# Kernel optimization log

Measured on AMD Instinct MI355X. Metric: run time of the kernel, lower is better.

Reference implementation:

```python
import jax, jax.numpy as jnp
import numpy as np

N = 100000       # nodes
DEG = 16         # in-degree per node
E = N * DEG      # edges
IN_DIM = 128
H_DIM = 128
NEG_SLOPE = 0.01  # F.leaky_relu default


def setup_inputs() -> dict:
    key = jax.random.key(0)
    ks = jax.random.split(key, 12)
    sc = 0.05
    attr = jax.random.normal(ks[0], (N, IN_DIM), jnp.float32)
    edge_d = jax.random.uniform(ks[1], (E, 1), dtype=jnp.float32)
    edge_src = jax.random.randint(ks[2], (E,), 0, N, dtype=jnp.int32)
    edge_dst = jnp.repeat(jnp.arange(N, dtype=jnp.int32), DEG)  # every node gets DEG msgs
    return {
        "attr": attr,
        "edge_d": edge_d,
        "W_V1": jax.random.normal(ks[3], (1, 1), jnp.float32) * sc,
        "W_W1": jax.random.normal(ks[4], (H_DIM, IN_DIM), jnp.float32) * sc,
        "W_U1": jax.random.normal(ks[5], (H_DIM, IN_DIM), jnp.float32) * sc,
        "W_a1": jax.random.normal(ks[6], (1, 2 * H_DIM + 1), jnp.float32) * sc,
        "W_V2": jax.random.normal(ks[7], (1, 1), jnp.float32) * sc,
        "W_W2": jax.random.normal(ks[8], (H_DIM, H_DIM), jnp.float32) * sc,
        "W_U2": jax.random.normal(ks[9], (H_DIM, H_DIM), jnp.float32) * sc,
        "W_a2": jax.random.normal(ks[10], (1, 2 * H_DIM + 1), jnp.float32) * sc,
        "edge_src": edge_src,
        "edge_dst": edge_dst,
    }


def gat_layer(h, edge_d, edge_src, edge_dst, W_V, W_W, W_U, W_a):
    n = h.shape[0]
    t = edge_d @ W_V.T                      # [E,1] edge feature transform (fcV)
    z = h @ W_W.T                           # [N,H] (fcW)
    z_i = h @ W_U.T                         # [N,H] (fcU)
    Hd = z.shape[1]
    a = W_a[0]                              # [2H+1]
    a_src, a_dst, a_t = a[:Hd], a[Hd:2 * Hd], a[2 * Hd:]
    # attn_fc(concat(z_src, z_dst, t)) decomposed into per-node scores + edge term
    s_src = z @ a_src                       # [N]
    s_dst = z @ a_dst                       # [N]
    e = s_src[edge_src] + s_dst[edge_dst] + (t @ a_t)  # [E]
    e = jax.nn.leaky_relu(e, NEG_SLOPE)
    # per-destination-node softmax over incoming edges (mailbox softmax)
    m = jax.ops.segment_max(e, edge_dst, num_segments=n)
    ex = jnp.exp(e - m[edge_dst])
    denom = jax.ops.segment_sum(ex, edge_dst, num_segments=n)
    alpha = ex / denom[edge_dst]            # [E]
    # weighted neighbor aggregation
    zn = jax.ops.segment_sum(alpha[:, None] * z[edge_src], edge_dst, num_segments=n)
    return jax.nn.relu(z_i + zn)


def reference(attr, edge_d, W_V1, W_W1, W_U1, W_a1, W_V2, W_W2, W_U2, W_a2,
              edge_src, edge_dst):
    h = gat_layer(attr, edge_d, edge_src, edge_dst, W_V1, W_W1, W_U1, W_a1)
    h = gat_layer(h, edge_d, edge_src, edge_dst, W_V2, W_W2, W_U2, W_a2)
    return h
```

## Files before the change

kernel.cpp:

```cpp
#include <hip/hip_runtime.h>

#define N_NODES 100000
#define DEG 16
#define DIM 128
#define NGROUPS 6250
#define GPB 5
#define DBLOCKS (NGROUPS / GPB)

typedef short bf16x8 __attribute__((ext_vector_type(8)));
typedef float f32x4 __attribute__((ext_vector_type(4)));

__device__ __forceinline__ unsigned short f2bf(float f) {
    unsigned int u = __builtin_bit_cast(unsigned int, f);
    u = (u + 0x7fffu + ((u >> 16) & 1u)) >> 16;
    return (unsigned short)u;
}
__device__ __forceinline__ float bf2f(unsigned short h) {
    unsigned int u = ((unsigned int)h) << 16;
    return __builtin_bit_cast(float, u);
}

template <bool F32IN>
__global__ __launch_bounds__(256) void dense_fused(
    const void* __restrict__ hsrc,
    const float* __restrict__ W_W,
    const float* __restrict__ W_U,
    const float* __restrict__ W_a,
    unsigned short* __restrict__ zcat,
    float* __restrict__ s_src,
    float* __restrict__ s_dst)
{
    __shared__ float sred[2][2][2][16];

    const int wave = threadIdx.x >> 6;
    const int lane = threadIdx.x & 63;
    const int n16 = lane & 15;
    const int quad = lane >> 4;

    const float* Wbase = (wave < 2) ? (W_W + (size_t)wave * 64 * DIM)
                                    : (W_U + (size_t)(wave - 2) * 64 * DIM);
    bf16x8 wfrag[4][4];
#pragma unroll
    for (int ct = 0; ct < 4; ct++) {
        const float* wrow = Wbase + (size_t)(ct * 16 + n16) * DIM + quad * 8;
#pragma unroll
        for (int ks = 0; ks < 4; ks++) {
            float4 lo = *(const float4*)(wrow + ks * 32);
            float4 hi = *(const float4*)(wrow + ks * 32 + 4);
            bf16x8 f;
            f[0] = (short)f2bf(lo.x); f[1] = (short)f2bf(lo.y);
            f[2] = (short)f2bf(lo.z); f[3] = (short)f2bf(lo.w);
            f[4] = (short)f2bf(hi.x); f[5] = (short)f2bf(hi.y);
            f[6] = (short)f2bf(hi.z); f[7] = (short)f2bf(hi.w);
            wfrag[ct][ks] = f;
        }
    }

    float4 av_s[4], av_d[4];
    if (wave < 2) {
#pragma unroll
        for (int ct = 0; ct < 4; ct++) {
            av_s[ct] = *(const float4*)(W_a + wave * 64 + ct * 16 + quad * 4);
            av_d[ct] = *(const float4*)(W_a + DIM + wave * 64 + ct * 16 + quad * 4);
        }
    }

    for (int g = 0; g < GPB; g++) {
        const int nodebase = (blockIdx.x * GPB + g) * 16;

        bf16x8 hfrag[4];
        if (F32IN) {
            const float* hrow = (const float*)hsrc + (size_t)(nodebase + n16) * DIM + quad * 8;
#pragma unroll
            for (int ks = 0; ks < 4; ks++) {
                float4 lo = *(const float4*)(hrow + ks * 32);
                float4 hi = *(const float4*)(hrow + ks * 32 + 4);
                bf16x8 f;
                f[0] = (short)f2bf(lo.x); f[1] = (short)f2bf(lo.y);
                f[2] = (short)f2bf(lo.z); f[3] = (short)f2bf(lo.w);
                f[4] = (short)f2bf(hi.x); f[5] = (short)f2bf(hi.y);
                f[6] = (short)f2bf(hi.z); f[7] = (short)f2bf(hi.w);
                hfrag[ks] = f;
            }
        } else {
            const unsigned short* hrow = (const unsigned short*)hsrc + (size_t)(nodebase + n16) * DIM + quad * 8;
#pragma unroll
            for (int ks = 0; ks < 4; ks++)
                hfrag[ks] = *(const bf16x8*)(hrow + ks * 32);
        }

        f32x4 acc[4];
#pragma unroll
        for (int ct = 0; ct < 4; ct++) {
            f32x4 a = {0.f, 0.f, 0.f, 0.f};
#pragma unroll
            for (int ks = 0; ks < 4; ks++)
                a = __builtin_amdgcn_mfma_f32_16x16x32_bf16(wfrag[ct][ks], hfrag[ks], a, 0, 0, 0);
            acc[ct] = a;
        }

        unsigned short* orow = zcat + (size_t)(nodebase + n16) * 256 + wave * 64 + quad * 4;
#pragma unroll
        for (int ct = 0; ct < 4; ct++) {
            uint2 pk;
            pk.x = (unsigned int)f2bf(acc[ct][0]) | ((unsigned int)f2bf(acc[ct][1]) << 16);
            pk.y = (unsigned int)f2bf(acc[ct][2]) | ((unsigned int)f2bf(acc[ct][3]) << 16);
            *(uint2*)(orow + ct * 16) = pk;
        }

        if (wave < 2) {
            float ps = 0.f, pd = 0.f;
#pragma unroll
            for (int ct = 0; ct < 4; ct++) {
                ps += acc[ct][0] * av_s[ct].x + acc[ct][1] * av_s[ct].y
                    + acc[ct][2] * av_s[ct].z + acc[ct][3] * av_s[ct].w;
                pd += acc[ct][0] * av_d[ct].x + acc[ct][1] * av_d[ct].y
                    + acc[ct][2] * av_d[ct].z + acc[ct][3] * av_d[ct].w;
            }
            ps += __shfl_xor(ps, 16); ps += __shfl_xor(ps, 32);
            pd += __shfl_xor(pd, 16); pd += __shfl_xor(pd, 32);
            if (lane < 16) {
                sred[g & 1][wave][0][n16] = ps;
                sred[g & 1][wave][1][n16] = pd;
            }
        }
        __syncthreads();
        if (wave == 3) {
            if (lane < 16)
                s_src[nodebase + lane] = sred[g & 1][0][0][lane] + sred[g & 1][1][0][lane];
            else if (lane < 32)
                s_dst[nodebase + lane - 16] = sred[g & 1][0][1][lane - 16] + sred[g & 1][1][1][lane - 16];
        }
    }
}

__global__ __launch_bounds__(256) void aggr_kernel(
    const unsigned short* __restrict__ zcat,
    const float* __restrict__ s_src,
    const float* __restrict__ s_dst,
    const float* __restrict__ edge_d,
    const int* __restrict__ edge_src,
    const float* __restrict__ W_V,
    const float* __restrict__ W_a,
    unsigned short* __restrict__ out_bf16,
    float* __restrict__ out_f32)
{
    __shared__ float alpha_s[16][DEG];
    __shared__ int   src_s[16][DEG];

    const int t = threadIdx.x;
    const int base = blockIdx.x * 16;

    {
        int nl = t >> 4, j = t & 15;
        int node = base + nl;
        int e = node * DEG + j;
        int s = edge_src[e];
        float coef = W_V[0] * W_a[2 * DIM];
        float x = s_src[s] + s_dst[node] + edge_d[e] * coef;
        x = x > 0.f ? x : 0.01f * x;
        float m = x;
        m = fmaxf(m, __shfl_xor(m, 1));
        m = fmaxf(m, __shfl_xor(m, 2));
        m = fmaxf(m, __shfl_xor(m, 4));
        m = fmaxf(m, __shfl_xor(m, 8));
        float ex = __expf(x - m);
        float d = ex;
        d += __shfl_xor(d, 1); d += __shfl_xor(d, 2);
        d += __shfl_xor(d, 4); d += __shfl_xor(d, 8);
        alpha_s[nl][j] = ex / d;
        src_s[nl][j] = s;
    }
    __syncthreads();

    const int nl = t >> 4;
    const int node = base + nl;
    const int c8 = (t & 15) * 8;

    float acc[8] = {};
#pragma unroll
    for (int j = 0; j < DEG; j++) {
        int s = src_s[nl][j];
        float a = alpha_s[nl][j];
        uint4 raw = *(const uint4*)(zcat + (size_t)s * 256 + c8);
        acc[0] += a * bf2f((unsigned short)raw.x);
        acc[1] += a * bf2f((unsigned short)(raw.x >> 16));
        acc[2] += a * bf2f((unsigned short)raw.y);
        acc[3] += a * bf2f((unsigned short)(raw.y >> 16));
        acc[4] += a * bf2f((unsigned short)raw.z);
        acc[5] += a * bf2f((unsigned short)(raw.z >> 16));
        acc[6] += a * bf2f((unsigned short)raw.w);
        acc[7] += a * bf2f((unsigned short)(raw.w >> 16));
    }

    uint4 zr = *(const uint4*)(zcat + (size_t)node * 256 + 128 + c8);
    float v[8];
    v[0] = fmaxf(bf2f((unsigned short)zr.x) + acc[0], 0.f);
    v[1] = fmaxf(bf2f((unsigned short)(zr.x >> 16)) + acc[1], 0.f);
    v[2] = fmaxf(bf2f((unsigned short)zr.y) + acc[2], 0.f);
    v[3] = fmaxf(bf2f((unsigned short)(zr.y >> 16)) + acc[3], 0.f);
    v[4] = fmaxf(bf2f((unsigned short)zr.z) + acc[4], 0.f);
    v[5] = fmaxf(bf2f((unsigned short)(zr.z >> 16)) + acc[5], 0.f);
    v[6] = fmaxf(bf2f((unsigned short)zr.w) + acc[6], 0.f);
    v[7] = fmaxf(bf2f((unsigned short)(zr.w >> 16)) + acc[7], 0.f);

    if (out_f32) {
        float* op = out_f32 + (size_t)node * DIM + c8;
        *(float4*)op       = make_float4(v[0], v[1], v[2], v[3]);
        *(float4*)(op + 4) = make_float4(v[4], v[5], v[6], v[7]);
    } else {
        uint4 pk;
        pk.x = (unsigned int)f2bf(v[0]) | ((unsigned int)f2bf(v[1]) << 16);
        pk.y = (unsigned int)f2bf(v[2]) | ((unsigned int)f2bf(v[3]) << 16);
        pk.z = (unsigned int)f2bf(v[4]) | ((unsigned int)f2bf(v[5]) << 16);
        pk.w = (unsigned int)f2bf(v[6]) | ((unsigned int)f2bf(v[7]) << 16);
        *(uint4*)(out_bf16 + (size_t)node * DIM + c8) = pk;
    }
}

extern "C" void kernel_launch(void* const* d_in, const int* in_sizes, int n_in,
                              void* d_out, int out_size, void* d_ws, size_t ws_size,
                              hipStream_t stream) {
    const float* attr     = (const float*)d_in[0];
    const float* edge_d   = (const float*)d_in[1];
    const float* W_V1     = (const float*)d_in[2];
    const float* W_W1     = (const float*)d_in[3];
    const float* W_U1     = (const float*)d_in[4];
    const float* W_a1     = (const float*)d_in[5];
    const float* W_V2     = (const float*)d_in[6];
    const float* W_W2     = (const float*)d_in[7];
    const float* W_U2     = (const float*)d_in[8];
    const float* W_a2     = (const float*)d_in[9];
    const int*   edge_src = (const int*)d_in[10];

    float* out = (float*)d_out;

    char* ws = (char*)d_ws;
    unsigned short* zcat = (unsigned short*)ws;
    unsigned short* h1   = (unsigned short*)(ws + 52u * 1024 * 1024);
    float* s_src         = (float*)(ws + 78u * 1024 * 1024);
    float* s_dst         = (float*)(ws + 79u * 1024 * 1024);

    dense_fused<true><<<DBLOCKS, 256, 0, stream>>>(attr, W_W1, W_U1, W_a1,
                                                   zcat, s_src, s_dst);
    aggr_kernel<<<NGROUPS, 256, 0, stream>>>(zcat, s_src, s_dst, edge_d, edge_src,
                                             W_V1, W_a1, h1, nullptr);

    dense_fused<false><<<DBLOCKS, 256, 0, stream>>>(h1, W_W2, W_U2, W_a2,
                                                    zcat, s_src, s_dst);
    aggr_kernel<<<NGROUPS, 256, 0, stream>>>(zcat, s_src, s_dst, edge_d, edge_src,
                                             W_V2, W_a2, nullptr, out);
}
```

Measured before the change: 333.6 us.

## Prefetch node tiles in dense kernel, drop block sync, batch gathers in aggregation

The dense kernel now loads the next group's input rows into registers while the current group's MFMAs run, double-buffering the fragments. It also removes the shared-memory reduction and __syncthreads by writing per-wave partial attention scores to separate arrays, which the aggregation kernel sums. The aggregation kernel issues all 16 neighbor gathers up front to expose memory-level parallelism, and both kernels get occupancy hints in launch_bounds. This raises register pressure and adds extra score arrays and reads in exchange for fewer stalls.

```diff
diff --git a/kernel.cpp b/kernel.cpp
--- a/kernel.cpp
+++ b/kernel.cpp
@@ -21,21 +21,20 @@
 }
 
 template <bool F32IN>
-__global__ __launch_bounds__(256) void dense_fused(
+__global__ __launch_bounds__(256, 2) void dense_fused(
     const void* __restrict__ hsrc,
     const float* __restrict__ W_W,
     const float* __restrict__ W_U,
     const float* __restrict__ W_a,
     unsigned short* __restrict__ zcat,
-    float* __restrict__ s_src,
-    float* __restrict__ s_dst)
+    float* __restrict__ s_src0, float* __restrict__ s_src1,
+    float* __restrict__ s_dst0, float* __restrict__ s_dst1)
 {
-    __shared__ float sred[2][2][2][16];
-
     const int wave = threadIdx.x >> 6;
     const int lane = threadIdx.x & 63;
     const int n16 = lane & 15;
     const int quad = lane >> 4;
+    const int gbase = blockIdx.x * GPB;
 
     const float* Wbase = (wave < 2) ? (W_W + (size_t)wave * 64 * DIM)
                                     : (W_U + (size_t)(wave - 2) * 64 * DIM);
@@ -56,38 +55,54 @@
         }
     }
 
-    float4 av_s[4], av_d[4];
-    if (wave < 2) {
-#pragma unroll
-        for (int ct = 0; ct < 4; ct++) {
-            av_s[ct] = *(const float4*)(W_a + wave * 64 + ct * 16 + quad * 4);
-            av_d[ct] = *(const float4*)(W_a + DIM + wave * 64 + ct * 16 + quad * 4);
-        }
-    }
-
-    for (int g = 0; g < GPB; g++) {
-        const int nodebase = (blockIdx.x * GPB + g) * 16;
-
-        bf16x8 hfrag[4];
-        if (F32IN) {
+    float4 rf[8];
+    bf16x8 rb[2][4];
+    bf16x8 hfragA[4], hfragB[4];
+
+    auto issue = [&](int g) {
+        int nodebase = (gbase + g) * 16;
+        if constexpr (F32IN) {
             const float* hrow = (const float*)hsrc + (size_t)(nodebase + n16) * DIM + quad * 8;
 #pragma unroll
             for (int ks = 0; ks < 4; ks++) {
-                float4 lo = *(const float4*)(hrow + ks * 32);
-                float4 hi = *(const float4*)(hrow + ks * 32 + 4);
+                rf[ks * 2]     = *(const float4*)(hrow + ks * 32);
+                rf[ks * 2 + 1] = *(const float4*)(hrow + ks * 32 + 4);
+            }
+        } else {
+            const unsigned short* hrow = (const unsigned short*)hsrc + (size_t)(nodebase + n16) * DIM + quad * 8;
+#pragma unroll
+            for (int ks = 0; ks < 4; ks++)
+                rb[g & 1][ks] = *(const bf16x8*)(hrow + ks * 32);
+        }
+    };
+    auto convert = [&](int g, bf16x8* dst) {
+        if constexpr (F32IN) {
+#pragma unroll
+            for (int ks = 0; ks < 4; ks++) {
+                float4 lo = rf[ks * 2], hi = rf[ks * 2 + 1];
                 bf16x8 f;
                 f[0] = (short)f2bf(lo.x); f[1] = (short)f2bf(lo.y);
                 f[2] = (short)f2bf(lo.z); f[3] = (short)f2bf(lo.w);
                 f[4] = (short)f2bf(hi.x); f[5] = (short)f2bf(hi.y);
                 f[6] = (short)f2bf(hi.z); f[7] = (short)f2bf(hi.w);
-                hfrag[ks] = f;
+                dst[ks] = f;
             }
         } else {
-            const unsigned short* hrow = (const unsigned short*)hsrc + (size_t)(nodebase + n16) * DIM + quad * 8;
-#pragma unroll
-            for (int ks = 0; ks < 4; ks++)
-                hfrag[ks] = *(const bf16x8*)(hrow + ks * 32);
-        }
+#pragma unroll
+            for (int ks = 0; ks < 4; ks++) dst[ks] = rb[g & 1][ks];
+        }
+    };
+
+    issue(0);
+    convert(0, hfragA);
+
+#pragma unroll
+    for (int g = 0; g < GPB; g++) {
+        const int nodebase = (gbase + g) * 16;
+        bf16x8* cur = (g & 1) ? hfragB : hfragA;
+        bf16x8* nxt = (g & 1) ? hfragA : hfragB;
+
+        if (g + 1 < GPB) issue(g + 1);
 
         f32x4 acc[4];
 #pragma unroll
@@ -95,7 +110,7 @@
             f32x4 a = {0.f, 0.f, 0.f, 0.f};
 #pragma unroll
             for (int ks = 0; ks < 4; ks++)
-                a = __builtin_amdgcn_mfma_f32_16x16x32_bf16(wfrag[ct][ks], hfrag[ks], a, 0, 0, 0);
+                a = __builtin_amdgcn_mfma_f32_16x16x32_bf16(wfrag[ct][ks], cur[ks], a, 0, 0, 0);
             acc[ct] = a;
         }
 
@@ -112,32 +127,31 @@
             float ps = 0.f, pd = 0.f;
 #pragma unroll
             for (int ct = 0; ct < 4; ct++) {
-                ps += acc[ct][0] * av_s[ct].x + acc[ct][1] * av_s[ct].y
-                    + acc[ct][2] * av_s[ct].z + acc[ct][3] * av_s[ct].w;
-                pd += acc[ct][0] * av_d[ct].x + acc[ct][1] * av_d[ct].y
-                    + acc[ct][2] * av_d[ct].z + acc[ct][3] * av_d[ct].w;
+                float4 as = *(const float4*)(W_a + wave * 64 + ct * 16 + quad * 4);
+                float4 ad = *(const float4*)(W_a + DIM + wave * 64 + ct * 16 + quad * 4);
+                ps += acc[ct][0] * as.x + acc[ct][1] * as.y
+                    + acc[ct][2] * as.z + acc[ct][3] * as.w;
+                pd += acc[ct][0] * ad.x + acc[ct][1] * ad.y
+                    + acc[ct][2] * ad.z + acc[ct][3] * ad.w;
             }
             ps += __shfl_xor(ps, 16); ps += __shfl_xor(ps, 32);
             pd += __shfl_xor(pd, 16); pd += __shfl_xor(pd, 32);
             if (lane < 16) {
-                sred[g & 1][wave][0][n16] = ps;
-                sred[g & 1][wave][1][n16] = pd;
-            }
-        }
-        __syncthreads();
-        if (wave == 3) {
-            if (lane < 16)
-                s_src[nodebase + lane] = sred[g & 1][0][0][lane] + sred[g & 1][1][0][lane];
-            else if (lane < 32)
-                s_dst[nodebase + lane - 16] = sred[g & 1][0][1][lane - 16] + sred[g & 1][1][1][lane - 16];
-        }
-    }
-}
-
-__global__ __launch_bounds__(256) void aggr_kernel(
+                float* sp = wave == 0 ? s_src0 : s_src1;
+                float* dp = wave == 0 ? s_dst0 : s_dst1;
+                sp[nodebase + lane] = ps;
+                dp[nodebase + lane] = pd;
+            }
+        }
+
+        if (g + 1 < GPB) convert(g + 1, nxt);
+    }
+}
+
+__global__ __launch_bounds__(256, 3) void aggr_kernel(
     const unsigned short* __restrict__ zcat,
-    const float* __restrict__ s_src,
-    const float* __restrict__ s_dst,
+    const float* __restrict__ s_src0, const float* __restrict__ s_src1,
+    const float* __restrict__ s_dst0, const float* __restrict__ s_dst1,
     const float* __restrict__ edge_d,
     const int* __restrict__ edge_src,
     const float* __restrict__ W_V,
@@ -157,7 +171,8 @@
         int e = node * DEG + j;
         int s = edge_src[e];
         float coef = W_V[0] * W_a[2 * DIM];
-        float x = s_src[s] + s_dst[node] + edge_d[e] * coef;
+        float x = (s_src0[s] + s_src1[s]) + (s_dst0[node] + s_dst1[node])
+                + edge_d[e] * coef;
         x = x > 0.f ? x : 0.01f * x;
         float m = x;
         m = fmaxf(m, __shfl_xor(m, 1));
@@ -177,23 +192,26 @@
     const int node = base + nl;
     const int c8 = (t & 15) * 8;
 
+    uint4 raw[DEG];
+#pragma unroll
+    for (int j = 0; j < DEG; j++)
+        raw[j] = *(const uint4*)(zcat + (size_t)src_s[nl][j] * 256 + c8);
+    uint4 zr = *(const uint4*)(zcat + (size_t)node * 256 + 128 + c8);
+
     float acc[8] = {};
 #pragma unroll
     for (int j = 0; j < DEG; j++) {
-        int s = src_s[nl][j];
         float a = alpha_s[nl][j];
-        uint4 raw = *(const uint4*)(zcat + (size_t)s * 256 + c8);
-        acc[0] += a * bf2f((unsigned short)raw.x);
-        acc[1] += a * bf2f((unsigned short)(raw.x >> 16));
-        acc[2] += a * bf2f((unsigned short)raw.y);
-        acc[3] += a * bf2f((unsigned short)(raw.y >> 16));
-        acc[4] += a * bf2f((unsigned short)raw.z);
-        acc[5] += a * bf2f((unsigned short)(raw.z >> 16));
-        acc[6] += a * bf2f((unsigned short)raw.w);
-        acc[7] += a * bf2f((unsigned short)(raw.w >> 16));
-    }
-
-    uint4 zr = *(const uint4*)(zcat + (size_t)node * 256 + 128 + c8);
+        acc[0] += a * bf2f((unsigned short)raw[j].x);
+        acc[1] += a * bf2f((unsigned short)(raw[j].x >> 16));
+        acc[2] += a * bf2f((unsigned short)raw[j].y);
+        acc[3] += a * bf2f((unsigned short)(raw[j].y >> 16));
+        acc[4] += a * bf2f((unsigned short)raw[j].z);
+        acc[5] += a * bf2f((unsigned short)(raw[j].z >> 16));
+        acc[6] += a * bf2f((unsigned short)raw[j].w);
+        acc[7] += a * bf2f((unsigned short)(raw[j].w >> 16));
+    }
+
     float v[8];
     v[0] = fmaxf(bf2f((unsigned short)zr.x) + acc[0], 0.f);
     v[1] = fmaxf(bf2f((unsigned short)(zr.x >> 16)) + acc[1], 0.f);
@@ -238,16 +256,18 @@
     char* ws = (char*)d_ws;
     unsigned short* zcat = (unsigned short*)ws;
     unsigned short* h1   = (unsigned short*)(ws + 52u * 1024 * 1024);
-    float* s_src         = (float*)(ws + 78u * 1024 * 1024);
-    float* s_dst         = (float*)(ws + 79u * 1024 * 1024);
-
-    dense_fused<true><<<DBLOCKS, 256, 0, stream>>>(attr, W_W1, W_U1, W_a1,
-                                                   zcat, s_src, s_dst);
-    aggr_kernel<<<NGROUPS, 256, 0, stream>>>(zcat, s_src, s_dst, edge_d, edge_src,
-                                             W_V1, W_a1, h1, nullptr);
-
-    dense_fused<false><<<DBLOCKS, 256, 0, stream>>>(h1, W_W2, W_U2, W_a2,
-                                                    zcat, s_src, s_dst);
-    aggr_kernel<<<NGROUPS, 256, 0, stream>>>(zcat, s_src, s_dst, edge_d, edge_src,
-                                             W_V2, W_a2, nullptr, out);
-}
+    float* s_src0        = (float*)(ws + 78u * 1024 * 1024);
+    float* s_src1        = (float*)(ws + 79u * 1024 * 1024);
+    float* s_dst0        = (float*)(ws + 80u * 1024 * 1024);
+    float* s_dst1        = (float*)(ws + 81u * 1024 * 1024);
+
+    dense_fused<true><<<DBLOCKS, 256, 0, stream>>>(attr, W_W1, W_U1, W_a1, zcat,
+                                                   s_src0, s_src1, s_dst0, s_dst1);
+    aggr_kernel<<<NGROUPS, 256, 0, stream>>>(zcat, s_src0, s_src1, s_dst0, s_dst1,
+                                             edge_d, edge_src, W_V1, W_a1, h1, nullptr);
+
+    dense_fused<false><<<DBLOCKS, 256, 0, stream>>>(h1, W_W2, W_U2, W_a2, zcat,
+                                                    s_src0, s_src1, s_dst0, s_dst1);
+    aggr_kernel<<<NGROUPS, 256, 0, stream>>>(zcat, s_src0, s_src1, s_dst0, s_dst1,
+                                             edge_d, edge_src, W_V2, W_a2, nullptr, out);
+}
```

Measured after the change: 342.6 us. 2.7% more time.
